# Kernel optimization log

Hardware: AMD Instinct MI355X
Metric: run time of the kernel (lower is better)

The kernel has to match this reference:

```python
import jax, jax.numpy as jnp
import numpy as np

V, E, H = 32000, 256, 512  # vocab, embedding_dim, hidden_size
B, S, T = 32, 64, 64       # batch, src_len, trg_len


def gru_step(h, x, W_ih, W_hh, b_ih, b_hh):
    # torch nn.GRU cell math; W_ih: [3H,E], W_hh: [3H,H], gate order r,z,n
    gi = x @ W_ih.T + b_ih        # [B,3H]
    gh = h @ W_hh.T + b_hh        # [B,3H]
    i_r, i_z, i_n = jnp.split(gi, 3, axis=-1)
    h_r, h_z, h_n = jnp.split(gh, 3, axis=-1)
    r = jax.nn.sigmoid(i_r + h_r)
    z = jax.nn.sigmoid(i_z + h_z)
    n = jnp.tanh(i_n + r * h_n)
    return (1.0 - z) * n + z * h


def setup_inputs() -> dict:
    key = jax.random.key(0)
    ks = jax.random.split(key, 16)
    u = lambda k, shape: jax.random.uniform(k, shape, jnp.float32, -0.1, 0.1)
    return {
        "src": jax.random.randint(ks[0], (B, S), 0, V),
        "trg": jax.random.randint(ks[1], (B, T), 0, V),
        "emb_enc": u(ks[2], (V, E)),
        "W_ih_enc": u(ks[3], (3 * H, E)),
        "W_hh_enc": u(ks[4], (3 * H, H)),
        "b_ih_enc": u(ks[5], (3 * H,)),
        "b_hh_enc": u(ks[6], (3 * H,)),
        "emb_dec": u(ks[7], (V, E)),
        "W_ih_dec": u(ks[8], (3 * H, E)),
        "W_hh_dec": u(ks[9], (3 * H, H)),
        "b_ih_dec": u(ks[10], (3 * H,)),
        "b_hh_dec": u(ks[11], (3 * H,)),
        "fc_W": u(ks[12], (V, H)),
        "fc_b": u(ks[13], (V,)),
    }


def reference(src, trg, emb_enc, W_ih_enc, W_hh_enc, b_ih_enc, b_hh_enc,
              emb_dec, W_ih_dec, W_hh_dec, b_ih_dec, b_hh_dec, fc_W, fc_b):
    # ----- Encoder: embed src, run GRU over time, return final hidden -----
    x_emb = emb_enc[src]                       # [B,S,E]
    h0 = jnp.zeros((B, H), jnp.float32)

    def enc_step(h, x_t):
        return gru_step(h, x_t, W_ih_enc, W_hh_enc, b_ih_enc, b_hh_enc), None

    h_enc, _ = jax.lax.scan(enc_step, h0, x_emb.transpose(1, 0, 2))  # [B,H]

    # ----- Decoder: teacher_forcing_ratio=1.0 -> inputs are trg[:, :-1] -----
    dec_in = emb_dec[trg[:, :-1]]              # [B,T-1,E]

    def dec_step(h, x_t):
        h2 = gru_step(h, x_t, W_ih_dec, W_hh_dec, b_ih_dec, b_hh_dec)
        logits = h2 @ fc_W.T + fc_b            # [B,V]
        return h2, logits

    _, logits = jax.lax.scan(dec_step, h_enc, dec_in.transpose(1, 0, 2))  # [T-1,B,V]

    # outputs[:, 0] stays zeros as in the original torch loop (range starts at 1)
    outputs = jnp.concatenate(
        [jnp.zeros((B, 1, V), jnp.float32), logits.transpose(1, 0, 2)], axis=1)
    return outputs
```

## Files before the change

kernel.cpp:

```cpp
#include <hip/hip_runtime.h>
#include <stdint.h>

constexpr int NB = 32, NS = 64, NT = 64, NV = 32000, NE = 256, NH = 512;
constexpr int RG = 64;
constexpr int UW = 16;
constexpr int BW = 16;
constexpr int GRW = 3 * UW;
constexpr int TSTEPS = NS + NT - 1;

typedef unsigned short u16;
typedef unsigned u32;
typedef unsigned long long u64;
typedef short bf16x8 __attribute__((ext_vector_type(8)));
typedef float f32x4  __attribute__((ext_vector_type(4)));
typedef unsigned u32x4 __attribute__((ext_vector_type(4)));

__device__ inline u16 f2bf(float f){
  unsigned int u = __float_as_uint(f);
  u = u + 0x7FFFu + ((u >> 16) & 1u);
  return (u16)(u >> 16);
}
__device__ inline float bf2f(u16 h){ return __uint_as_float(((unsigned)h) << 16); }

__device__ inline void gload_lds16(const u16* g, u16* l){
  __builtin_amdgcn_global_load_lds((const __attribute__((address_space(1))) void*)g,
                                   (__attribute__((address_space(3))) void*)l, 16, 0, 0);
}

__device__ inline int ldsW_off(int r, int k16){
  return (k16 >> 2) * 3072 + ((r >> 4) << 10) + (((((k16 & 3) << 4)) | (r & 15)) << 4);
}
__device__ inline int ldsH_off(int r, int k16){
  return ((k16 >> 2) << 10) + (((((k16 & 3) << 4)) | r) << 4);
}

__device__ inline void load_h128(const u32* p, u32x4 v[8]){
  asm volatile(
    "global_load_dwordx4 %0, %8, off sc0 sc1\n\t"
    "global_load_dwordx4 %1, %8, off offset:16 sc0 sc1\n\t"
    "global_load_dwordx4 %2, %8, off offset:32 sc0 sc1\n\t"
    "global_load_dwordx4 %3, %8, off offset:48 sc0 sc1\n\t"
    "global_load_dwordx4 %4, %8, off offset:64 sc0 sc1\n\t"
    "global_load_dwordx4 %5, %8, off offset:80 sc0 sc1\n\t"
    "global_load_dwordx4 %6, %8, off offset:96 sc0 sc1\n\t"
    "global_load_dwordx4 %7, %8, off offset:112 sc0 sc1\n\t"
    "s_waitcnt vmcnt(0)"
    : "=&v"(v[0]), "=&v"(v[1]), "=&v"(v[2]), "=&v"(v[3]),
      "=&v"(v[4]), "=&v"(v[5]), "=&v"(v[6]), "=&v"(v[7])
    : "v"(p)
    : "memory");
}

__global__ void zero_init(float* __restrict__ out, u16* __restrict__ xdecpad, u16* __restrict__ hallpad,
                          u32* __restrict__ Hpk, u32* __restrict__ flags){
  int i = blockIdx.x * blockDim.x + threadIdx.x, st = gridDim.x * blockDim.x;
  for (int idx = i; idx < NB * NV; idx += st){
    int b = idx / NV, v = idx - b * NV;
    out[(size_t)b * NT * NV + v] = 0.f;
  }
  for (int idx = i; idx < 32 * NE; idx += st) xdecpad[idx] = 0;
  for (int idx = i; idx < 32 * NH; idx += st) hallpad[idx] = 0;
  for (int idx = i; idx < 2 * NB * NH; idx += st) Hpk[idx] = 0;
  for (int idx = i; idx < 1024; idx += st) flags[idx] = 0;
}

__global__ void cvt_f32_bf16(const float* __restrict__ in, u16* __restrict__ out, int n4){
  int i = blockIdx.x * blockDim.x + threadIdx.x, st = gridDim.x * blockDim.x;
  for (int idx = i; idx < n4; idx += st){
    float4 v = ((const float4*)in)[idx];
    unsigned lo = (unsigned)f2bf(v.x) | ((unsigned)f2bf(v.y) << 16);
    unsigned hi = (unsigned)f2bf(v.z) | ((unsigned)f2bf(v.w) << 16);
    *(uint2*)(out + (size_t)idx * 4) = make_uint2(lo, hi);
  }
}

__global__ void cvt_hilo(const float* __restrict__ in, u16* __restrict__ hi, u16* __restrict__ lo, int n){
  int i = blockIdx.x * blockDim.x + threadIdx.x, st = gridDim.x * blockDim.x;
  for (int idx = i; idx < n; idx += st){
    float w = in[idx];
    u16 h = f2bf(w);
    hi[idx] = h;
    lo[idx] = f2bf(w - bf2f(h));
  }
}

__global__ void embed_k(const int* __restrict__ idx, int ld, int tcount,
                        const float* __restrict__ emb, u16* __restrict__ xbf){
  int tid = blockIdx.x * blockDim.x + threadIdx.x;
  int n4 = tcount * NB * (NE / 4);
  if (tid >= n4) return;
  int e4 = tid & (NE/4 - 1);
  int m  = tid >> 6;
  int t = m / NB, b = m % NB;
  int row = idx[b * ld + t];
  float4 v = ((const float4*)(emb + (size_t)row * NE))[e4];
  unsigned lo = (unsigned)f2bf(v.x) | ((unsigned)f2bf(v.y) << 16);
  unsigned hi = (unsigned)f2bf(v.z) | ((unsigned)f2bf(v.w) << 16);
  *(uint2*)(xbf + (size_t)m * NE + e4 * 4) = make_uint2(lo, hi);
}

template<int KDIM, int MODE>
__global__ __launch_bounds__(256) void gemm_bt(const u16* __restrict__ A,
                                               const u16* __restrict__ Bm,
                                               const float* __restrict__ bias,
                                               float* __restrict__ C,
                                               int Mstore, int Nld)
{
  __shared__ u16 As[128 * 32];
  __shared__ u16 Bs[128 * 32];
  const int id = blockIdx.x;
  const int q = gridDim.x >> 3;
  const int wg = (id & 7) * q + (id >> 3);
  const int m0 = (wg & 15) * 128, n0 = (wg >> 4) * 128;
  const int tid  = threadIdx.x;
  const int lane = tid & 63;
  const int w = tid >> 6, wm = w >> 1, wn = w & 1;
  f32x4 acc[4][4] = {};

  const int sr = w * 16 + (lane >> 2);
  const int sc = (lane & 3) * 8;
  const u16* aS = A  + (size_t)(m0 + sr) * KDIM + sc;
  const u16* bS = Bm + (size_t)(n0 + sr) * KDIM + sc;
  u16* asl = As + w * 16 * 32;
  u16* bsl = Bs + w * 16 * 32;

  for (int k0 = 0; k0 < KDIM; k0 += 32){
    gload_lds16(aS + k0, asl);
    gload_lds16(aS + (size_t)64 * KDIM + k0, asl + 64 * 32);
    gload_lds16(bS + k0, bsl);
    gload_lds16(bS + (size_t)64 * KDIM + k0, bsl + 64 * 32);
    __syncthreads();
    bf16x8 af[4], bfr[4];
    #pragma unroll
    for (int i = 0; i < 4; ++i)
      af[i] = *(const bf16x8*)((const char*)As + (wm*64 + i*16 + (lane & 15)) * 64 + (lane >> 4) * 16);
    #pragma unroll
    for (int j = 0; j < 4; ++j)
      bfr[j] = *(const bf16x8*)((const char*)Bs + (wn*64 + j*16 + (lane & 15)) * 64 + (lane >> 4) * 16);
    #pragma unroll
    for (int i = 0; i < 4; ++i)
      #pragma unroll
      for (int j = 0; j < 4; ++j)
        acc[i][j] = __builtin_amdgcn_mfma_f32_16x16x32_bf16(af[i], bfr[j], acc[i][j], 0, 0, 0);
    __syncthreads();
  }

  #pragma unroll
  for (int i = 0; i < 4; ++i){
    #pragma unroll
    for (int j = 0; j < 4; ++j){
      int col = n0 + wn*64 + j*16 + (lane & 15);
      float bv = bias[col];
      #pragma unroll
      for (int rr = 0; rr < 4; ++rr){
        int row = m0 + wm*64 + i*16 + (lane >> 4) * 4 + rr;
        float val = acc[i][j][rr] + bv;
        int t_ = row >> 5, b_ = row & 31;
        if (MODE == 1){
          if (row < Mstore)
            C[(size_t)b_ * (NT * NV) + (size_t)(t_ + 1) * NV + col] = val;
        } else {
          C[((size_t)t_ * 1536 + col) * 32 + b_] = val;
        }
      }
    }
  }
}

__global__ __launch_bounds__(256) void gru_rec(
    const u16* __restrict__ WhiE, const u16* __restrict__ WloE,
    const u16* __restrict__ WhiD, const u16* __restrict__ WloD,
    const float* __restrict__ bhhE, const float* __restrict__ bhhD,
    const float* __restrict__ giTe, const float* __restrict__ giTd,
    u32* __restrict__ Hpk,
    u32* __restrict__ flags,
    u16* __restrict__ Hall)
{
  extern __shared__ char smem[];
  u16* Whi = (u16*)smem;
  u16* Wlo = Whi + GRW * NH;
  u16* Hhi = Wlo + GRW * NH;
  u16* Hlo = Hhi + BW * NH;
  float* GH = (float*)(Hlo + BW * NH);

  const int tid  = threadIdx.x;
  const int lane = tid & 63;
  const int w    = tid >> 6;
  const int bg   = blockIdx.x >> 5;
  const int ug   = blockIdx.x & 31;
  const int j0   = ug * UW;
  const int b0   = bg * BW;
  const unsigned myid = blockIdx.x;

  const int gu = tid >> 4, gb2 = tid & 15;
  const int jg = j0 + gu;
  const int bglob = b0 + gb2;
  const float beR = bhhE[jg], beZ = bhhE[NH + jg], beN = bhhE[2*NH + jg];
  const float bdR = bhhD[jg], bdZ = bhhD[NH + jg], bdN = bhhD[2*NH + jg];

  auto stageW = [&](const u16* Hi, const u16* Lo){
    for (int c = tid; c < GRW * 64; c += 256){
      int r = c >> 6, k16 = c & 63;
      int grow = (r >> 4) * NH + j0 + (r & 15);
      int d = ldsW_off(r, k16);
      *(uint4*)((char*)Whi + d) = *(const uint4*)(Hi + (size_t)grow * NH + k16 * 8);
      *(uint4*)((char*)Wlo + d) = *(const uint4*)(Lo + (size_t)grow * NH + k16 * 8);
    }
  };
  stageW(WhiE, WloE);

  const int srl = tid >> 4;
  const int sqq = tid & 15;

  for (int t = 0; t < TSTEPS; ++t){
    const bool dec = (t >= NS);
    __syncthreads();
    if (tid == 0 && t > 0)
      __hip_atomic_store(&flags[myid * 4], (u32)t, __ATOMIC_RELAXED, __HIP_MEMORY_SCOPE_AGENT);
    if (t == NS) stageW(WhiD, WloD);

    {
      int spins = 0;
      const int fl = (bg << 5) + (lane & 31);
      while (true){
        u32 f = __hip_atomic_load(&flags[fl * 4], __ATOMIC_RELAXED, __HIP_MEMORY_SCOPE_AGENT);
        if (__all((int)(lane >= 32 || (lane & 31) == ug || f >= (u32)t))) break;
        __builtin_amdgcn_s_sleep(1);
        if (++spins > (1 << 18)) break;
      }
    }

    {
      const u32* Hq = Hpk + (size_t)(t & 1) * NB * NH;
      u32x4 v[8];
      load_h128(Hq + (size_t)(b0 + srl) * NH + sqq * 32, v);
      #pragma unroll
      for (int i = 0; i < 4; ++i){
        u32x4 a = v[2*i], b2 = v[2*i+1];
        uint4 hw = make_uint4((a[0] & 0xffffu) | (a[1] << 16), (a[2] & 0xffffu) | (a[3] << 16),
                              (b2[0] & 0xffffu) | (b2[1] << 16), (b2[2] & 0xffffu) | (b2[3] << 16));
        uint4 lw = make_uint4((a[0] >> 16) | (a[1] & 0xffff0000u), (a[2] >> 16) | (a[3] & 0xffff0000u),
                              (b2[0] >> 16) | (b2[1] & 0xffff0000u), (b2[2] >> 16) | (b2[3] & 0xffff0000u));
        int d = ldsH_off(srl, sqq * 4 + i);
        *(uint4*)((char*)Hhi + d) = hw;
        *(uint4*)((char*)Hlo + d) = lw;
      }
    }
    __syncthreads();

    const float* gT = dec ? (giTd + (size_t)(t - NS) * 1536 * 32)
                          : (giTe + (size_t)t * 1536 * 32);
    float gr = gT[(size_t)(0 * NH + jg) * 32 + bglob];
    float gz = gT[(size_t)(1 * NH + jg) * 32 + bglob];
    float gn = gT[(size_t)(2 * NH + jg) * 32 + bglob];

    if (w < 3){
      f32x4 acc0 = {0.f,0.f,0.f,0.f}, acc1 = {0.f,0.f,0.f,0.f};
      const int ab = w * 1024 + lane * 16;
      const int bb = lane * 16;
      #pragma unroll
      for (int kk = 0; kk < 16; kk += 2){
        bf16x8 ah0 = *(const bf16x8*)((const char*)Whi + kk * 3072 + ab);
        bf16x8 al0 = *(const bf16x8*)((const char*)Wlo + kk * 3072 + ab);
        bf16x8 bh0 = *(const bf16x8*)((const char*)Hhi + kk * 1024 + bb);
        bf16x8 bl0 = *(const bf16x8*)((const char*)Hlo + kk * 1024 + bb);
        acc0 = __builtin_amdgcn_mfma_f32_16x16x32_bf16(ah0, bh0, acc0, 0, 0, 0);
        acc0 = __builtin_amdgcn_mfma_f32_16x16x32_bf16(al0, bh0, acc0, 0, 0, 0);
        acc0 = __builtin_amdgcn_mfma_f32_16x16x32_bf16(ah0, bl0, acc0, 0, 0, 0);
        bf16x8 ah1 = *(const bf16x8*)((const char*)Whi + (kk+1) * 3072 + ab);
        bf16x8 al1 = *(const bf16x8*)((const char*)Wlo + (kk+1) * 3072 + ab);
        bf16x8 bh1 = *(const bf16x8*)((const char*)Hhi + (kk+1) * 1024 + bb);
        bf16x8 bl1 = *(const bf16x8*)((const char*)Hlo + (kk+1) * 1024 + bb);
        acc1 = __builtin_amdgcn_mfma_f32_16x16x32_bf16(ah1, bh1, acc1, 0, 0, 0);
        acc1 = __builtin_amdgcn_mfma_f32_16x16x32_bf16(al1, bh1, acc1, 0, 0, 0);
        acc1 = __builtin_amdgcn_mfma_f32_16x16x32_bf16(ah1, bl1, acc1, 0, 0, 0);
      }
      f32x4 accs = acc0 + acc1;
      int col = lane & 15;
      #pragma unroll
      for (int r2 = 0; r2 < 4; ++r2){
        int row = w * 16 + ((lane >> 4) << 2) + r2;
        GH[row * BW + col] = accs[r2];
      }
    }
    __syncthreads();

    {
      float ghr = GH[(0 * UW + gu) * BW + gb2] + (dec ? bdR : beR);
      float ghz = GH[(1 * UW + gu) * BW + gb2] + (dec ? bdZ : beZ);
      float ghn = GH[(2 * UW + gu) * BW + gb2] + (dec ? bdN : beN);
      float r = 1.f / (1.f + expf(-(gr + ghr)));
      float z = 1.f / (1.f + expf(-(gz + ghz)));
      float n = tanhf(gn + r * ghn);
      int coff = ldsH_off(gb2, jg >> 3) + (jg & 7) * 2;
      float hp = bf2f(*(const u16*)((char*)Hhi + coff))
               + bf2f(*(const u16*)((char*)Hlo + coff));
      float hnew = (1.f - z) * n + z * hp;
      u16 hi = f2bf(hnew);
      u16 lo = f2bf(hnew - bf2f(hi));
      if (dec) Hall[((size_t)(t - NS) * NB + bglob) * NH + jg] = hi;
      if (t < TSTEPS - 1){
        __hip_atomic_store(&Hpk[((size_t)((t + 1) & 1) * NB + bglob) * NH + jg],
                           (u32)hi | ((u32)lo << 16),
                           __ATOMIC_RELAXED, __HIP_MEMORY_SCOPE_AGENT);
      }
    }
  }
}

extern "C" void kernel_launch(void* const* d_in, const int* in_sizes, int n_in,
                              void* d_out, int out_size, void* d_ws, size_t ws_size,
                              hipStream_t stream)
{
  const int*   src      = (const int*)  d_in[0];
  const int*   trg      = (const int*)  d_in[1];
  const float* emb_enc  = (const float*)d_in[2];
  const float* W_ih_enc = (const float*)d_in[3];
  const float* W_hh_enc = (const float*)d_in[4];
  const float* b_ih_enc = (const float*)d_in[5];
  const float* b_hh_enc = (const float*)d_in[6];
  const float* emb_dec  = (const float*)d_in[7];
  const float* W_ih_dec = (const float*)d_in[8];
  const float* W_hh_dec = (const float*)d_in[9];
  const float* b_ih_dec = (const float*)d_in[10];
  const float* b_hh_dec = (const float*)d_in[11];
  const float* fc_W     = (const float*)d_in[12];
  const float* fc_b     = (const float*)d_in[13];
  float* out = (float*)d_out;

  char* ws = (char*)d_ws;
  size_t o = 0;
  auto alloc = [&](size_t bytes){ size_t r = o; o += (bytes + 255) & ~(size_t)255; return r; };
  u16*   xenc  = (u16*)(ws + alloc((size_t)2048 * NE * 2));
  u16*   xdec  = (u16*)(ws + alloc((size_t)2048 * NE * 2));
  u16*   wihe  = (u16*)(ws + alloc((size_t)3 * NH * NE * 2));
  u16*   wihd  = (u16*)(ws + alloc((size_t)3 * NH * NE * 2));
  u16*   fcWbf = (u16*)(ws + alloc((size_t)NV * NH * 2));
  u16*   whiE  = (u16*)(ws + alloc((size_t)3 * NH * NH * 2));
  u16*   wloE  = (u16*)(ws + alloc((size_t)3 * NH * NH * 2));
  u16*   whiD  = (u16*)(ws + alloc((size_t)3 * NH * NH * 2));
  u16*   wloD  = (u16*)(ws + alloc((size_t)3 * NH * NH * 2));
  float* gie   = (float*)(ws + alloc((size_t)2048 * 3 * NH * 4));
  float* gid   = (float*)(ws + alloc((size_t)2048 * 3 * NH * 4));
  u32*   Hpk   = (u32*)(ws + alloc((size_t)2 * NB * NH * 4));
  u32*   flags = (u32*)(ws + alloc(4096));
  u16*   Hall  = (u16*)(ws + alloc((size_t)2048 * NH * 2));

  zero_init<<<256, 256, 0, stream>>>(out, xdec + (size_t)2016 * NE, Hall + (size_t)2016 * NH, Hpk, flags);
  cvt_f32_bf16<<<384, 256, 0, stream>>>(W_ih_enc, wihe, 3*NH*NE/4);
  cvt_f32_bf16<<<384, 256, 0, stream>>>(W_ih_dec, wihd, 3*NH*NE/4);
  cvt_f32_bf16<<<2048, 256, 0, stream>>>(fc_W, fcWbf, NV*NH/4);
  cvt_hilo<<<1024, 256, 0, stream>>>(W_hh_enc, whiE, wloE, 3*NH*NH);
  cvt_hilo<<<1024, 256, 0, stream>>>(W_hh_dec, whiD, wloD, 3*NH*NH);
  embed_k<<<(NS*NB*64 + 255)/256, 256, 0, stream>>>(src, NS, NS, emb_enc, xenc);
  embed_k<<<((NT-1)*NB*64 + 255)/256, 256, 0, stream>>>(trg, NT, NT-1, emb_dec, xdec);

  gemm_bt<NE, 2><<<192, 256, 0, stream>>>(xenc, wihe, b_ih_enc, gie, 2048, 0);
  gemm_bt<NE, 2><<<192, 256, 0, stream>>>(xdec, wihd, b_ih_dec, gid, 2048, 0);

  constexpr int SMEM_BYTES = 2 * (GRW * NH * 2) + 2 * (BW * NH * 2) + GRW * BW * 4;
  static_assert(SMEM_BYTES <= 160 * 1024, "LDS over 160 KiB");
  static_assert(SMEM_BYTES == 134144, "unexpected LDS size");
  (void)hipFuncSetAttribute(reinterpret_cast<const void*>(&gru_rec),
                            hipFuncAttributeMaxDynamicSharedMemorySize, SMEM_BYTES);
  gru_rec<<<RG, 256, SMEM_BYTES, stream>>>(whiE, wloE, whiD, wloD, b_hh_enc, b_hh_dec,
                                           gie, gid, Hpk, flags, Hall);

  gemm_bt<NH, 1><<<4000, 256, 0, stream>>>(Hall, fcWbf, fc_b, out, 2016, 0);
}
```

Before: 779.5 us.

## Double-buffer GEMM LDS tiles and XOR-swizzle the hidden-state LDS layout

The bf16 GEMM kernel now keeps two LDS stages. It issues the global-to-LDS loads for the next K tile before running the MFMAs on the current tile, so load latency overlaps compute. This doubles the GEMM's shared memory footprint, which may cut occupancy. Separately, the recurrent kernel's hidden-state LDS layout is XOR-swizzled by K-group on both the write offset and the MFMA operand reads, aiming to reduce LDS bank conflicts during the per-step h writes.

```diff
diff --git a/kernel.cpp b/kernel.cpp
--- a/kernel.cpp
+++ b/kernel.cpp
@@ -31,7 +31,8 @@
   return (k16 >> 2) * 3072 + ((r >> 4) << 10) + (((((k16 & 3) << 4)) | (r & 15)) << 4);
 }
 __device__ inline int ldsH_off(int r, int k16){
-  return ((k16 >> 2) << 10) + (((((k16 & 3) << 4)) | r) << 4);
+  int base = ((k16 >> 2) << 10) + (((((k16 & 3) << 4)) | r) << 4);
+  return base ^ (((base >> 10) & 15) << 4);
 }
 
 __device__ inline void load_h128(const u32* p, u32x4 v[8]){
@@ -106,8 +107,8 @@
                                                float* __restrict__ C,
                                                int Mstore, int Nld)
 {
-  __shared__ u16 As[128 * 32];
-  __shared__ u16 Bs[128 * 32];
+  __shared__ u16 As[2 * 128 * 32];
+  __shared__ u16 Bs[2 * 128 * 32];
   const int id = blockIdx.x;
   const int q = gridDim.x >> 3;
   const int wg = (id & 7) * q + (id >> 3);
@@ -124,19 +125,29 @@
   u16* asl = As + w * 16 * 32;
   u16* bsl = Bs + w * 16 * 32;
 
-  for (int k0 = 0; k0 < KDIM; k0 += 32){
-    gload_lds16(aS + k0, asl);
-    gload_lds16(aS + (size_t)64 * KDIM + k0, asl + 64 * 32);
-    gload_lds16(bS + k0, bsl);
-    gload_lds16(bS + (size_t)64 * KDIM + k0, bsl + 64 * 32);
-    __syncthreads();
+  auto STAGE = [&](int p, int k0){
+    u16* ad = asl + p * 4096;
+    u16* bd = bsl + p * 4096;
+    gload_lds16(aS + k0, ad);
+    gload_lds16(aS + (size_t)64 * KDIM + k0, ad + 64 * 32);
+    gload_lds16(bS + k0, bd);
+    gload_lds16(bS + (size_t)64 * KDIM + k0, bd + 64 * 32);
+  };
+
+  constexpr int NK = KDIM / 32;
+  STAGE(0, 0);
+  __syncthreads();
+  for (int t2 = 0; t2 < NK; ++t2){
+    if (t2 + 1 < NK) STAGE((t2 + 1) & 1, (t2 + 1) * 32);
+    const char* Ab = (const char*)As + (t2 & 1) * 8192;
+    const char* Bb = (const char*)Bs + (t2 & 1) * 8192;
     bf16x8 af[4], bfr[4];
     #pragma unroll
     for (int i = 0; i < 4; ++i)
-      af[i] = *(const bf16x8*)((const char*)As + (wm*64 + i*16 + (lane & 15)) * 64 + (lane >> 4) * 16);
+      af[i] = *(const bf16x8*)(Ab + (wm*64 + i*16 + (lane & 15)) * 64 + (lane >> 4) * 16);
     #pragma unroll
     for (int j = 0; j < 4; ++j)
-      bfr[j] = *(const bf16x8*)((const char*)Bs + (wn*64 + j*16 + (lane & 15)) * 64 + (lane >> 4) * 16);
+      bfr[j] = *(const bf16x8*)(Bb + (wn*64 + j*16 + (lane & 15)) * 64 + (lane >> 4) * 16);
     #pragma unroll
     for (int i = 0; i < 4; ++i)
       #pragma unroll
@@ -260,17 +271,19 @@
       const int bb = lane * 16;
       #pragma unroll
       for (int kk = 0; kk < 16; kk += 2){
+        const int bx0 = kk * 1024 + (bb ^ ((kk & 15) << 4));
+        const int bx1 = (kk+1) * 1024 + (bb ^ (((kk+1) & 15) << 4));
         bf16x8 ah0 = *(const bf16x8*)((const char*)Whi + kk * 3072 + ab);
         bf16x8 al0 = *(const bf16x8*)((const char*)Wlo + kk * 3072 + ab);
-        bf16x8 bh0 = *(const bf16x8*)((const char*)Hhi + kk * 1024 + bb);
-        bf16x8 bl0 = *(const bf16x8*)((const char*)Hlo + kk * 1024 + bb);
+        bf16x8 bh0 = *(const bf16x8*)((const char*)Hhi + bx0);
+        bf16x8 bl0 = *(const bf16x8*)((const char*)Hlo + bx0);
         acc0 = __builtin_amdgcn_mfma_f32_16x16x32_bf16(ah0, bh0, acc0, 0, 0, 0);
         acc0 = __builtin_amdgcn_mfma_f32_16x16x32_bf16(al0, bh0, acc0, 0, 0, 0);
         acc0 = __builtin_amdgcn_mfma_f32_16x16x32_bf16(ah0, bl0, acc0, 0, 0, 0);
         bf16x8 ah1 = *(const bf16x8*)((const char*)Whi + (kk+1) * 3072 + ab);
         bf16x8 al1 = *(const bf16x8*)((const char*)Wlo + (kk+1) * 3072 + ab);
-        bf16x8 bh1 = *(const bf16x8*)((const char*)Hhi + (kk+1) * 1024 + bb);
-        bf16x8 bl1 = *(const bf16x8*)((const char*)Hlo + (kk+1) * 1024 + bb);
+        bf16x8 bh1 = *(const bf16x8*)((const char*)Hhi + bx1);
+        bf16x8 bl1 = *(const bf16x8*)((const char*)Hlo + bx1);
         acc1 = __builtin_amdgcn_mfma_f32_16x16x32_bf16(ah1, bh1, acc1, 0, 0, 0);
         acc1 = __builtin_amdgcn_mfma_f32_16x16x32_bf16(al1, bh1, acc1, 0, 0, 0);
         acc1 = __builtin_amdgcn_mfma_f32_16x16x32_bf16(ah1, bl1, acc1, 0, 0, 0);
```

Result: no change. 789.8 us (+1.3%).
